# Performance work log

Hardware: AMD Instinct MI355X
Metric: run time of the kernel (lower is better)

Reference implementation:

```python
import jax, jax.numpy as jnp
import numpy as np

N_NODES = 1_000_000
N_EDGES = 4_000_000  # knn_k = 4
N_GRAPHS = 1024
HIDDEN = 64
N_FEAT = 4


def setup_inputs() -> dict:
    key = jax.random.key(0)
    k0, k1, k2, k3, k4 = jax.random.split(key, 5)
    x = jax.random.normal(k0, (N_NODES, N_FEAT), dtype=jnp.float32)
    edge_index = jax.random.randint(k1, (2, N_EDGES), 0, N_NODES, dtype=jnp.int64)
    batch = jnp.sort(jax.random.randint(k2, (N_NODES,), 0, N_GRAPHS, dtype=jnp.int64))
    W1 = jax.random.normal(k3, (N_FEAT, HIDDEN), dtype=jnp.float32) * 0.5
    b1 = jnp.zeros((HIDDEN,), dtype=jnp.float32)
    W2 = jax.random.normal(k4, (HIDDEN, 1), dtype=jnp.float32) * 0.1
    b2 = jnp.zeros((1,), dtype=jnp.float32)
    return {"x": x, "W1": W1, "b1": b1, "W2": W2, "b2": b2,
            "edge_index": edge_index, "batch": batch}


def gcn_conv(x, edge_index, W, b):
    # PyG GCNConv: linear transform, add self-loops, sym-normalize, scatter-add.
    n = x.shape[0]
    h = x @ W  # [N, 64]
    loop = jnp.arange(n, dtype=edge_index.dtype)
    row = jnp.concatenate([edge_index[0], loop])  # source j
    col = jnp.concatenate([edge_index[1], loop])  # target i
    deg = jax.ops.segment_sum(jnp.ones_like(col, dtype=h.dtype), col, num_segments=n)
    dis = jnp.where(deg > 0, jax.lax.rsqrt(jnp.maximum(deg, 1.0)), 0.0)
    norm = dis[row] * dis[col]  # [E+N]
    out = jax.ops.segment_sum(h[row] * norm[:, None], col, num_segments=n)
    return out + b


def reference(x, W1, b1, W2, b2, edge_index, batch):
    h = gcn_conv(x, edge_index, W1, b1)          # [N, 64]
    h = jax.nn.elu(h)                            # ELU activation
    pooled = jax.ops.segment_sum(h, batch, num_segments=N_GRAPHS)  # global_add_pool
    return pooled @ W2 + b2                      # [G, 1]
```

## Files before the change

### kernel.cpp

```cpp
#include <hip/hip_runtime.h>
#include <hip/hip_fp16.h>

#define N_NODES 1000000
#define N_EDGES 4000000
#define N_GRAPHS 1024
#define HIDDEN 64

#define G1 250
#define T1 512
#define EPB (N_EDGES / G1)
#define EPB4 (EPB / 4)
#define BSHIFT 10
#define BSIZE 1024
#define NBK 1024
#define NBUCK ((N_NODES + BSIZE - 1) / BSIZE)

__global__ __launch_bounds__(T1) void k_hist(const int4* __restrict__ col4,
                                             int* __restrict__ part,
                                             float* __restrict__ out,
                                             const float* __restrict__ b2) {
    __shared__ int h[NBK];
    int t = threadIdx.x, blk = blockIdx.x;
    for (int i = t; i < NBK; i += T1) h[i] = 0;
    int gid = blk * T1 + t;
    if (gid < N_GRAPHS) out[gid] = b2[0];
    __syncthreads();
    int b0 = blk * EPB4;
    for (int i = t; i < EPB4; i += T1) {
        int4 c = col4[b0 + i];
        atomicAdd(&h[((unsigned)c.x) >> BSHIFT], 1);
        atomicAdd(&h[((unsigned)c.y) >> BSHIFT], 1);
        atomicAdd(&h[((unsigned)c.z) >> BSHIFT], 1);
        atomicAdd(&h[((unsigned)c.w) >> BSHIFT], 1);
    }
    __syncthreads();
    for (int i = t; i < NBK; i += T1) part[blk * NBK + i] = h[i];
}

__global__ __launch_bounds__(1024) void k_off(int* __restrict__ part,
                                              int* __restrict__ ebase,
                                              int* __restrict__ ecnt) {
    __shared__ int sc[NBK];
    int b = threadIdx.x;
    int run = 0;
    for (int k = 0; k < G1; ++k) {
        int v = part[k * NBK + b];
        part[k * NBK + b] = run;
        run += v;
    }
    ecnt[b] = run;
    int run4 = (run + 3) & ~3;
    sc[b] = run4;
    __syncthreads();
    for (int o = 1; o < NBK; o <<= 1) {
        int v = (b >= o) ? sc[b - o] : 0;
        __syncthreads();
        sc[b] += v;
        __syncthreads();
    }
    int base = sc[b] - run4;
    ebase[b] = base;
    for (int k = 0; k < G1; ++k) part[k * NBK + b] += base;
}

__global__ __launch_bounds__(T1) void k_part(const int4* __restrict__ row4,
                                             const int4* __restrict__ col4,
                                             const int* __restrict__ part,
                                             unsigned* __restrict__ epair) {
    __shared__ int cur[NBK];
    int t = threadIdx.x, blk = blockIdx.x;
    for (int i = t; i < NBK; i += T1) cur[i] = part[blk * NBK + i];
    __syncthreads();
    int b0 = blk * EPB4;
    for (int i = t; i < EPB4; i += T1) {
        int4 c = col4[b0 + i];
        int4 r = row4[b0 + i];
        int cc[4] = {c.x, c.y, c.z, c.w};
        int rr[4] = {r.x, r.y, r.z, r.w};
        #pragma unroll
        for (int k = 0; k < 4; ++k) {
            int b = ((unsigned)cc[k]) >> BSHIFT;
            int pos = atomicAdd(&cur[b], 1);
            epair[pos] = ((unsigned)(cc[k] & (BSIZE - 1)) << 20) | (unsigned)rr[k];
        }
    }
}

__global__ __launch_bounds__(512) void k_deg2(const unsigned* __restrict__ epair,
                                              const int* __restrict__ ebase,
                                              const int* __restrict__ ecnt,
                                              const float4* __restrict__ x,
                                              float* __restrict__ dis,
                                              uint2* __restrict__ xdh) {
    __shared__ int deg[BSIZE];
    int t = threadIdx.x, b = blockIdx.x;
    for (int i = t; i < BSIZE; i += 512) deg[i] = 1;
    __syncthreads();
    int ne = ecnt[b];
    const unsigned* ep = epair + ebase[b];
    int ne4 = ne & ~3;
    for (int i = 4 * t; i < ne4; i += 2048) {
        uint4 u = *(const uint4*)(ep + i);
        atomicAdd(&deg[u.x >> 20], 1);
        atomicAdd(&deg[u.y >> 20], 1);
        atomicAdd(&deg[u.z >> 20], 1);
        atomicAdd(&deg[u.w >> 20], 1);
    }
    for (int i = ne4 + t; i < ne; i += 512) atomicAdd(&deg[ep[i] >> 20], 1);
    __syncthreads();
    int n0 = b << BSHIFT;
    for (int i = t; i < BSIZE; i += 512) {
        int node = n0 + i;
        if (node < N_NODES) {
            float d = rsqrtf((float)deg[i]);
            dis[node] = d;
            float4 xv = x[node];
            __half2 h01 = __floats2half2_rn(xv.x * d, xv.y * d);
            __half2 h23 = __floats2half2_rn(xv.z * d, xv.w * d);
            uint2 pk;
            pk.x = *(unsigned*)&h01;
            pk.y = *(unsigned*)&h23;
            xdh[node] = pk;
        }
    }
}

__device__ __forceinline__ void acc_edge(unsigned u, uint2 p, float* sf) {
    int loc = u >> 20;
    __half2 h01 = *(__half2*)&p.x;
    __half2 h23 = *(__half2*)&p.y;
    float2 f01 = __half22float2(h01);
    float2 f23 = __half22float2(h23);
    float* sp = sf + loc * 5;
    atomicAdd(sp + 0, f01.x);
    atomicAdd(sp + 1, f01.y);
    atomicAdd(sp + 2, f23.x);
    atomicAdd(sp + 3, f23.y);
}

__global__ __launch_bounds__(512) void k_accF(const unsigned* __restrict__ epair,
                                              const int* __restrict__ ebase,
                                              const int* __restrict__ ecnt,
                                              const uint2* __restrict__ xdh,
                                              const float* __restrict__ dis,
                                              const int* __restrict__ batch,
                                              const float* __restrict__ W1,
                                              const float* __restrict__ b1,
                                              const float* __restrict__ W2,
                                              float* __restrict__ out) {
    __shared__ float sf[BSIZE * 5];
    int t = threadIdx.x, b = blockIdx.x;
    for (int i = t; i < BSIZE * 5; i += 512) sf[i] = 0.f;
    __syncthreads();
    int ne = ecnt[b];
    const unsigned* ep = epair + ebase[b];
    int ne8 = ne & ~7;
    for (int i = 8 * t; i < ne8; i += 4096) {
        uint4 q0 = *(const uint4*)(ep + i);
        uint4 q1 = *(const uint4*)(ep + i + 4);
        uint2 p0 = xdh[q0.x & 0xFFFFFu];
        uint2 p1 = xdh[q0.y & 0xFFFFFu];
        uint2 p2 = xdh[q0.z & 0xFFFFFu];
        uint2 p3 = xdh[q0.w & 0xFFFFFu];
        uint2 p4 = xdh[q1.x & 0xFFFFFu];
        uint2 p5 = xdh[q1.y & 0xFFFFFu];
        uint2 p6 = xdh[q1.z & 0xFFFFFu];
        uint2 p7 = xdh[q1.w & 0xFFFFFu];
        acc_edge(q0.x, p0, sf);
        acc_edge(q0.y, p1, sf);
        acc_edge(q0.z, p2, sf);
        acc_edge(q0.w, p3, sf);
        acc_edge(q1.x, p4, sf);
        acc_edge(q1.y, p5, sf);
        acc_edge(q1.z, p6, sf);
        acc_edge(q1.w, p7, sf);
    }
    for (int i = ne8 + t; i < ne; i += 512) {
        unsigned u = ep[i];
        acc_edge(u, xdh[u & 0xFFFFFu], sf);
    }
    __syncthreads();
    int n0 = b << BSHIFT;
    #pragma unroll
    for (int k = 0; k < BSIZE / 512; ++k) {
        int ln = t + k * 512;
        int node = n0 + ln;
        bool valid = node < N_NODES;
        float acc = 0.f;
        int g = -1;
        if (valid) {
            const float* sp = sf + ln * 5;
            uint2 p = xdh[node];
            __half2 h01 = *(__half2*)&p.x;
            __half2 h23 = *(__half2*)&p.y;
            float2 f01 = __half22float2(h01);
            float2 f23 = __half22float2(h23);
            float d = dis[node];
            float u0 = d * (sp[0] + f01.x);
            float u1 = d * (sp[1] + f01.y);
            float u2 = d * (sp[2] + f23.x);
            float u3 = d * (sp[3] + f23.y);
            g = batch[node];
            #pragma unroll
            for (int kk = 0; kk < HIDDEN; ++kk) {
                float tt = fmaf(u0, W1[kk],
                           fmaf(u1, W1[HIDDEN + kk],
                           fmaf(u2, W1[2 * HIDDEN + kk],
                           fmaf(u3, W1[3 * HIDDEN + kk], b1[kk]))));
                float h = tt > 0.f ? tt : (__expf(tt) - 1.f);
                acc = fmaf(h, W2[kk], acc);
            }
        }
        unsigned long long rem = __ballot(valid);
        while (rem) {
            int leader = __ffsll(rem) - 1;
            int gl = __shfl(g, leader);
            bool mine = valid && (g == gl);
            unsigned long long mask = __ballot(mine);
            float v = mine ? acc : 0.f;
            #pragma unroll
            for (int o = 32; o; o >>= 1) v += __shfl_xor(v, o);
            if ((int)(t & 63) == leader) unsafeAtomicAdd(&out[gl], v);
            rem &= ~mask;
        }
    }
}

__global__ __launch_bounds__(256) void k_init(int* __restrict__ deg, float4* __restrict__ s,
                                              float* __restrict__ out, const float* __restrict__ b2) {
    int i = blockIdx.x * blockDim.x + threadIdx.x;
    if (i < N_NODES) { deg[i] = 1; s[i] = make_float4(0.f, 0.f, 0.f, 0.f); }
    if (i < N_GRAPHS) out[i] = b2[0];
}
__global__ __launch_bounds__(256) void k_deg(const int* __restrict__ col, int* __restrict__ deg) {
    int e = blockIdx.x * blockDim.x + threadIdx.x;
    if (e < N_EDGES) atomicAdd(&deg[col[e]], 1);
}
__global__ __launch_bounds__(256) void k_dis(const int* __restrict__ deg, float* __restrict__ dis) {
    int i = blockIdx.x * blockDim.x + threadIdx.x;
    if (i < N_NODES) dis[i] = rsqrtf((float)deg[i]);
}
__global__ __launch_bounds__(256) void k_scatter(const int* __restrict__ row, const int* __restrict__ col,
                                                 const float4* __restrict__ x, const float* __restrict__ dis,
                                                 float* __restrict__ s) {
    int e = blockIdx.x * blockDim.x + threadIdx.x;
    if (e >= N_EDGES) return;
    int j = row[e], i = col[e];
    float dj = dis[j];
    float4 xj = x[j];
    float* sp = s + 4ll * (long long)i;
    unsafeAtomicAdd(sp + 0, xj.x * dj);
    unsafeAtomicAdd(sp + 1, xj.y * dj);
    unsafeAtomicAdd(sp + 2, xj.z * dj);
    unsafeAtomicAdd(sp + 3, xj.w * dj);
}
__global__ __launch_bounds__(256) void k_node(const float4* __restrict__ x, const float4* __restrict__ s,
                                              const float* __restrict__ dis, const int* __restrict__ batch,
                                              const float* __restrict__ W1, const float* __restrict__ b1,
                                              const float* __restrict__ W2, float* __restrict__ out) {
    int n = blockIdx.x * blockDim.x + threadIdx.x;
    bool valid = n < N_NODES;
    float acc = 0.f; int g = -1;
    if (valid) {
        float4 xn = x[n], sn = s[n];
        float di = dis[n], inv = di * di;
        float u0 = di * sn.x + inv * xn.x, u1 = di * sn.y + inv * xn.y;
        float u2 = di * sn.z + inv * xn.z, u3 = di * sn.w + inv * xn.w;
        g = batch[n];
        #pragma unroll
        for (int k = 0; k < HIDDEN; ++k) {
            float t = fmaf(u0, W1[k], fmaf(u1, W1[HIDDEN + k],
                      fmaf(u2, W1[2 * HIDDEN + k], fmaf(u3, W1[3 * HIDDEN + k], b1[k]))));
            float h = t > 0.f ? t : expm1f(t);
            acc = fmaf(h, W2[k], acc);
        }
    }
    unsigned long long rem = __ballot(valid);
    while (rem) {
        int leader = __ffsll(rem) - 1;
        int gl = __shfl(g, leader);
        bool mine = valid && (g == gl);
        unsigned long long mask = __ballot(mine);
        float v = mine ? acc : 0.f;
        #pragma unroll
        for (int o = 32; o; o >>= 1) v += __shfl_xor(v, o);
        if ((int)(threadIdx.x & 63) == leader) unsafeAtomicAdd(&out[gl], v);
        rem &= ~mask;
    }
}

extern "C" void kernel_launch(void* const* d_in, const int* in_sizes, int n_in,
                              void* d_out, int out_size, void* d_ws, size_t ws_size,
                              hipStream_t stream) {
    const float* x   = (const float*)d_in[0];
    const float* W1  = (const float*)d_in[1];
    const float* b1  = (const float*)d_in[2];
    const float* W2  = (const float*)d_in[3];
    const float* b2  = (const float*)d_in[4];
    const int*   ei  = (const int*)d_in[5];
    const int*   bat = (const int*)d_in[6];
    float* out = (float*)d_out;

    const int* row = ei;
    const int* col = ei + N_EDGES;
    char* ws = (char*)d_ws;

    size_t o_ep   = 0;
    size_t o_xdh  = o_ep + (size_t)(N_EDGES + 4 * NBK) * 4;
    size_t o_dis  = o_xdh + (size_t)N_NODES * 8;
    size_t o_part = o_dis + (size_t)N_NODES * 4;
    size_t o_eb   = o_part + (size_t)G1 * NBK * 4;
    size_t o_ec   = o_eb + NBK * 4;
    size_t need   = o_ec + NBK * 4;

    if (ws_size >= need) {
        unsigned* epair = (unsigned*)(ws + o_ep);
        uint2*    xdh   = (uint2*)(ws + o_xdh);
        float*    dis   = (float*)(ws + o_dis);
        int*      part  = (int*)(ws + o_part);
        int*      ebase = (int*)(ws + o_eb);
        int*      ecnt  = (int*)(ws + o_ec);

        k_hist<<<G1, T1, 0, stream>>>((const int4*)col, part, out, b2);
        k_off<<<1, 1024, 0, stream>>>(part, ebase, ecnt);
        k_part<<<G1, T1, 0, stream>>>((const int4*)row, (const int4*)col, part, epair);
        k_deg2<<<NBUCK, 512, 0, stream>>>(epair, ebase, ecnt, (const float4*)x, dis, xdh);
        k_accF<<<NBUCK, 512, 0, stream>>>(epair, ebase, ecnt, xdh, dis, bat, W1, b1, W2, out);
    } else {
        int nb_n = (N_NODES + 255) / 256;
        int nb_e = (N_EDGES + 255) / 256;
        int*    deg = (int*)(ws);
        float*  dis = (float*)(ws + (size_t)N_NODES * 4);
        float*  s   = (float*)(ws + (size_t)N_NODES * 8);
        float4* s4  = (float4*)s;
        k_init<<<nb_n, 256, 0, stream>>>(deg, s4, out, b2);
        k_deg<<<nb_e, 256, 0, stream>>>(col, deg);
        k_dis<<<nb_n, 256, 0, stream>>>(deg, dis);
        k_scatter<<<nb_e, 256, 0, stream>>>(row, col, (const float4*)x, dis, s);
        k_node<<<nb_n, 256, 0, stream>>>((const float4*)x, s4, dis, bat, W1, b1, W2, out);
    }
}
```

Baseline: 202.1 us.

## Parallelize bucket offset scan across blocks and use nontemporal streaming loads

The single-block offset kernel, which walked 250 partial histograms serially per bucket, is split in two. One kernel runs 1024 blocks that each scan one bucket column. A second single-block kernel scans the bucket totals, and the partition kernel now adds the bucket base when it loads its cursors. Separately, streaming reads of edge indices, packed edge pairs and node features switch to nontemporal loads so they pollute the cache less. The cost is one extra kernel launch, and nontemporal hints could hurt if the data would have been reused from cache.

```diff
diff --git a/kernel.cpp b/kernel.cpp
--- a/kernel.cpp
+++ b/kernel.cpp
@@ -14,6 +14,23 @@
 #define BSIZE 1024
 #define NBK 1024
 #define NBUCK ((N_NODES + BSIZE - 1) / BSIZE)
+
+typedef int   vi4 __attribute__((ext_vector_type(4)));
+typedef unsigned vu4 __attribute__((ext_vector_type(4)));
+typedef float vf4 __attribute__((ext_vector_type(4)));
+
+__device__ __forceinline__ int4 nt_int4(const int4* p) {
+    vi4 v = __builtin_nontemporal_load((const vi4*)p);
+    return make_int4(v.x, v.y, v.z, v.w);
+}
+__device__ __forceinline__ uint4 nt_uint4(const uint4* p) {
+    vu4 v = __builtin_nontemporal_load((const vu4*)p);
+    return make_uint4(v.x, v.y, v.z, v.w);
+}
+__device__ __forceinline__ float4 nt_float4(const float4* p) {
+    vf4 v = __builtin_nontemporal_load((const vf4*)p);
+    return make_float4(v.x, v.y, v.z, v.w);
+}
 
 __global__ __launch_bounds__(T1) void k_hist(const int4* __restrict__ col4,
                                              int* __restrict__ part,
@@ -27,7 +44,7 @@
     __syncthreads();
     int b0 = blk * EPB4;
     for (int i = t; i < EPB4; i += T1) {
-        int4 c = col4[b0 + i];
+        int4 c = nt_int4(col4 + b0 + i);
         atomicAdd(&h[((unsigned)c.x) >> BSHIFT], 1);
         atomicAdd(&h[((unsigned)c.y) >> BSHIFT], 1);
         atomicAdd(&h[((unsigned)c.z) >> BSHIFT], 1);
@@ -37,19 +54,29 @@
     for (int i = t; i < NBK; i += T1) part[blk * NBK + i] = h[i];
 }
 
-__global__ __launch_bounds__(1024) void k_off(int* __restrict__ part,
-                                              int* __restrict__ ebase,
-                                              int* __restrict__ ecnt) {
+__global__ __launch_bounds__(256) void k_colscan(int* __restrict__ part,
+                                                 int* __restrict__ ecnt) {
+    int b = blockIdx.x;
+    int t = threadIdx.x;
+    __shared__ int a[256];
+    int v = (t < G1) ? part[t * NBK + b] : 0;
+    a[t] = v;
+    __syncthreads();
+    for (int o = 1; o < 256; o <<= 1) {
+        int u = (t >= o) ? a[t - o] : 0;
+        __syncthreads();
+        a[t] += u;
+        __syncthreads();
+    }
+    if (t < G1) part[t * NBK + b] = a[t] - v;
+    if (t == 255) ecnt[b] = a[255];
+}
+
+__global__ __launch_bounds__(NBK) void k_bscan(const int* __restrict__ ecnt,
+                                               int* __restrict__ ebase) {
     __shared__ int sc[NBK];
     int b = threadIdx.x;
-    int run = 0;
-    for (int k = 0; k < G1; ++k) {
-        int v = part[k * NBK + b];
-        part[k * NBK + b] = run;
-        run += v;
-    }
-    ecnt[b] = run;
-    int run4 = (run + 3) & ~3;
+    int run4 = (ecnt[b] + 3) & ~3;
     sc[b] = run4;
     __syncthreads();
     for (int o = 1; o < NBK; o <<= 1) {
@@ -58,23 +85,22 @@
         sc[b] += v;
         __syncthreads();
     }
-    int base = sc[b] - run4;
-    ebase[b] = base;
-    for (int k = 0; k < G1; ++k) part[k * NBK + b] += base;
+    ebase[b] = sc[b] - run4;
 }
 
 __global__ __launch_bounds__(T1) void k_part(const int4* __restrict__ row4,
                                              const int4* __restrict__ col4,
                                              const int* __restrict__ part,
+                                             const int* __restrict__ ebase,
                                              unsigned* __restrict__ epair) {
     __shared__ int cur[NBK];
     int t = threadIdx.x, blk = blockIdx.x;
-    for (int i = t; i < NBK; i += T1) cur[i] = part[blk * NBK + i];
+    for (int i = t; i < NBK; i += T1) cur[i] = part[blk * NBK + i] + ebase[i];
     __syncthreads();
     int b0 = blk * EPB4;
     for (int i = t; i < EPB4; i += T1) {
-        int4 c = col4[b0 + i];
-        int4 r = row4[b0 + i];
+        int4 c = nt_int4(col4 + b0 + i);
+        int4 r = nt_int4(row4 + b0 + i);
         int cc[4] = {c.x, c.y, c.z, c.w};
         int rr[4] = {r.x, r.y, r.z, r.w};
         #pragma unroll
@@ -100,7 +126,7 @@
     const unsigned* ep = epair + ebase[b];
     int ne4 = ne & ~3;
     for (int i = 4 * t; i < ne4; i += 2048) {
-        uint4 u = *(const uint4*)(ep + i);
+        uint4 u = nt_uint4((const uint4*)(ep + i));
         atomicAdd(&deg[u.x >> 20], 1);
         atomicAdd(&deg[u.y >> 20], 1);
         atomicAdd(&deg[u.z >> 20], 1);
@@ -114,7 +140,7 @@
         if (node < N_NODES) {
             float d = rsqrtf((float)deg[i]);
             dis[node] = d;
-            float4 xv = x[node];
+            float4 xv = nt_float4(x + node);
             __half2 h01 = __floats2half2_rn(xv.x * d, xv.y * d);
             __half2 h23 = __floats2half2_rn(xv.z * d, xv.w * d);
             uint2 pk;
@@ -156,8 +182,8 @@
     const unsigned* ep = epair + ebase[b];
     int ne8 = ne & ~7;
     for (int i = 8 * t; i < ne8; i += 4096) {
-        uint4 q0 = *(const uint4*)(ep + i);
-        uint4 q1 = *(const uint4*)(ep + i + 4);
+        uint4 q0 = nt_uint4((const uint4*)(ep + i));
+        uint4 q1 = nt_uint4((const uint4*)(ep + i + 4));
         uint2 p0 = xdh[q0.x & 0xFFFFFu];
         uint2 p1 = xdh[q0.y & 0xFFFFFu];
         uint2 p2 = xdh[q0.z & 0xFFFFFu];
@@ -322,8 +348,9 @@
         int*      ecnt  = (int*)(ws + o_ec);
 
         k_hist<<<G1, T1, 0, stream>>>((const int4*)col, part, out, b2);
-        k_off<<<1, 1024, 0, stream>>>(part, ebase, ecnt);
-        k_part<<<G1, T1, 0, stream>>>((const int4*)row, (const int4*)col, part, epair);
+        k_colscan<<<NBK, 256, 0, stream>>>(part, ecnt);
+        k_bscan<<<1, NBK, 0, stream>>>(ecnt, ebase);
+        k_part<<<G1, T1, 0, stream>>>((const int4*)row, (const int4*)col, part, ebase, epair);
         k_deg2<<<NBUCK, 512, 0, stream>>>(epair, ebase, ecnt, (const float4*)x, dis, xdh);
         k_accF<<<NBUCK, 512, 0, stream>>>(epair, ebase, ecnt, xdh, dis, bat, W1, b1, W2, out);
     } else {
```

After: 189.8 us. 6.1% less time.
